# Kernel tuning notes

Hardware: AMD Instinct MI355X
Metric: run time of the kernel (lower is better)

The kernel has to match this reference:

```python
import jax, jax.numpy as jnp
import numpy as np

B, DIN, H, NACT = 8192, 1025, 1024, 1026
NHEAD = 513  # npatches + STOP
K = 32       # kR = kS


def _make_seq(key, batch, n, k):
    k_idx, k_len = jax.random.split(key)
    # distinct indices per row: top-k of a random permutation
    perm = jnp.argsort(jax.random.uniform(k_idx, (batch, n)), axis=1)[:, :k]
    seq_len = jax.random.randint(k_len, (batch,), 1, k + 1).astype(jnp.int32)
    mask = jnp.arange(k)[None, :] < seq_len[:, None]
    seq_idx = jnp.where(mask, perm, -1).astype(jnp.int32)
    return seq_idx, seq_len


def setup_inputs() -> dict:
    key = jax.random.key(0)
    ks = jax.random.split(key, 8)
    state = jax.random.normal(ks[0], (B, DIN), dtype=jnp.float32)
    W0 = jax.random.normal(ks[1], (DIN, H), dtype=jnp.float32) * (2.0 / DIN) ** 0.5
    b0 = jnp.zeros((H,), jnp.float32)
    W1 = jax.random.normal(ks[2], (H, H), dtype=jnp.float32) * (2.0 / H) ** 0.5
    b1 = jnp.zeros((H,), jnp.float32)
    W2 = jax.random.normal(ks[3], (H, NACT), dtype=jnp.float32) * 0.01
    b2 = jnp.zeros((NACT,), jnp.float32)
    seq_idx_R, seq_len_R = _make_seq(ks[4], B, NHEAD, K)
    seq_idx_S, seq_len_S = _make_seq(ks[5], B, NHEAD, K)
    return {"state": state, "W0": W0, "b0": b0, "W1": W1, "b1": b1,
            "W2": W2, "b2": b2,
            "seq_idx_R": seq_idx_R, "seq_len_R": seq_len_R,
            "seq_idx_S": seq_idx_S, "seq_len_S": seq_len_S}


def _mlp(state, W0, b0, W1, b1, W2, b2):
    h = jax.nn.relu(state @ W0 + b0)
    h = jax.nn.relu(h @ W1 + b1)
    return h @ W2 + b2  # (B, NACT) logits


def _logprob_entropy_wo_replacement(logits, seq_idx, seq_len):
    # Faithful vectorized version of logprob_entropy_wo_replacement_batched.
    bsz, n = logits.shape
    col = jnp.arange(n)[None, :]
    neg_inf = jnp.float32(-jnp.inf)

    def step(carry, xs):
        remaining, logp, ent = carry          # (B,N) bool, (B,), (B,)
        t, idx_t = xs                          # scalar, (B,)
        active = t < seq_len                   # (B,)
        masked_logits = jnp.where(remaining, logits, neg_inf)
        lp = jax.nn.log_softmax(masked_logits, axis=-1)
        p = jnp.exp(lp)
        mp = jnp.where(remaining, p, 0.0)
        mlp_ = jnp.where(remaining, lp, 0.0)
        ent_step = -jnp.sum(mp * mlp_, axis=-1)
        ent = ent + jnp.where(active, ent_step, 0.0)
        valid = active & (idx_t >= 0)
        idx_safe = jnp.where(valid, idx_t, 0)
        g = jnp.take_along_axis(lp, idx_safe[:, None], axis=1)[:, 0]
        logp = logp + jnp.where(valid, g, 0.0)
        hit = (col == idx_safe[:, None]) & valid[:, None]
        remaining = remaining & ~hit
        return (remaining, logp, ent), None

    init = (jnp.ones((bsz, n), bool), jnp.zeros((bsz,), jnp.float32),
            jnp.zeros((bsz,), jnp.float32))
    ts = jnp.arange(seq_idx.shape[1], dtype=jnp.int32)
    (_, logp, ent), _ = jax.lax.scan(step, init, (ts, seq_idx.T))
    return logp, ent


def reference(state, W0, b0, W1, b1, W2, b2,
              seq_idx_R, seq_len_R, seq_idx_S, seq_len_S):
    x = _mlp(state, W0, b0, W1, b1, W2, b2)
    logpR, entR = _logprob_entropy_wo_replacement(x[:, :NHEAD], seq_idx_R, seq_len_R)
    logpS, entS = _logprob_entropy_wo_replacement(x[:, NHEAD:NHEAD + NHEAD], seq_idx_S, seq_len_S)
    # rows: [total logprob, total entropy] as in get_log_prob's (logpR+logpS, entR+entS)
    return jnp.stack([logpR + logpS, entR + entS], axis=0)  # (2, B)
```

## Files before the change

kernel.cpp:

```cpp
#include <hip/hip_runtime.h>
#include <cstdint>
#include <cstddef>

#define BATCH 8192
#define DIN   1025
#define HID   1024
#define NACT  1026
#define NHEAD 513
#define KSEL  32
#define KP0   1088
#define LGN   1024

typedef unsigned short u16;
typedef short bf16x8 __attribute__((ext_vector_type(8)));
typedef float f32x4 __attribute__((ext_vector_type(4)));

__device__ __forceinline__ u16 f2bf(float f) {
  unsigned u = __float_as_uint(f);
  u += 0x7fff + ((u >> 16) & 1);
  return (u16)(u >> 16);
}
__device__ __forceinline__ float bf2f(u16 h) {
  return __uint_as_float((unsigned)h << 16);
}

__device__ __forceinline__ void async_cp16(const u16* g, u16* l) {
  __builtin_amdgcn_global_load_lds((const __attribute__((address_space(1))) void*)g,
                                   (__attribute__((address_space(3))) void*)l,
                                   16, 0, 0);
}

__global__ __launch_bounds__(512) void k_cvt(const float* __restrict__ state,
    const float* __restrict__ W0, const float* __restrict__ W1,
    const float* __restrict__ W2,
    u16* __restrict__ As, u16* __restrict__ W0t, u16* __restrict__ W1t,
    u16* __restrict__ W2t, u16* __restrict__ W2c) {
  const int tid = threadIdx.x;
  const int b = blockIdx.x;
  {
    int i = b * 512 + tid;
    const int QPR = KP0 / 4;
    int r = i / QPR, c4 = (i - r * QPR) * 4;
    const float* src = state + (size_t)r * DIN + c4;
    ushort4 o;
    if (c4 + 3 < DIN) {
      o.x = f2bf(src[0]); o.y = f2bf(src[1]); o.z = f2bf(src[2]); o.w = f2bf(src[3]);
    } else {
      o.x = (c4 + 0 < DIN) ? f2bf(src[0]) : 0;
      o.y = (c4 + 1 < DIN) ? f2bf(src[1]) : 0;
      o.z = (c4 + 2 < DIN) ? f2bf(src[2]) : 0;
      o.w = (c4 + 3 < DIN) ? f2bf(src[3]) : 0;
    }
    *(ushort4*)(As + (size_t)r * KP0 + c4) = o;
  }
  if (b >= 3137) return;
  if (b == 3136) {
    for (int e = tid; e < 2048; e += 512) {
      int j = e >> 10, k = e & 1023;
      W2c[e] = f2bf(W2[(size_t)k * NACT + 1024 + j]);
    }
    return;
  }
  const float* W; u16* Wt; int K, ldW, Kp, tt = b;
  if (tt < 1088)      { W = W0; Wt = W0t; K = DIN; ldW = HID;  Kp = KP0; }
  else if (tt < 2112) { tt -= 1088; W = W1; Wt = W1t; K = HID; ldW = HID;  Kp = HID; }
  else                { tt -= 2112; W = W2; Wt = W2t; K = HID; ldW = NACT; Kp = HID; }
  int n0 = (tt & 31) * 32, k0 = (tt >> 5) * 32;
  __shared__ float tile[32][33];
  const int tx = tid & 31, ty = tid >> 5;
#pragma unroll
  for (int i = 0; i < 32; i += 16) {
    int k = k0 + ty + i;
    tile[ty + i][tx] = (k < K) ? W[(size_t)k * ldW + n0 + tx] : 0.f;
  }
  __syncthreads();
#pragma unroll
  for (int i = 0; i < 32; i += 16)
    Wt[(size_t)(n0 + ty + i) * Kp + k0 + tx] = f2bf(tile[tx][ty + i]);
}

template<bool RELU, int K>
__global__ __launch_bounds__(256, 2)
void gemm_bt(const u16* __restrict__ A, const u16* __restrict__ Bt,
             const float* __restrict__ bias, u16* __restrict__ Cout, int ldc)
{
  __shared__ __align__(16) u16 lds[32768];

  const int d     = blockIdx.x;
  const int m8    = d & 7;
  const int ntile = (d >> 3) & 7;
  const int mtile = ((d >> 6) << 3) | m8;
  const size_t bm = (size_t)mtile * 128;
  const size_t bn = (size_t)ntile * 128;

  const int tid  = threadIdx.x;
  const int wave = tid >> 6;
  const int lane = tid & 63;
  const int waveM = wave >> 1, waveN = wave & 1;
  const int lr = lane & 15, lq = lane >> 4;

  const int row0 = tid >> 3;
  const int g_   = (tid & 7) ^ ((tid >> 3) & 7);
  const u16* gA0 = A  + (bm + row0)      * (size_t)K + g_ * 8;
  const u16* gA1 = A  + (bm + row0 + 32) * (size_t)K + g_ * 8;
  const u16* gA2 = A  + (bm + row0 + 64) * (size_t)K + g_ * 8;
  const u16* gA3 = A  + (bm + row0 + 96) * (size_t)K + g_ * 8;
  const u16* gB0 = Bt + (bn + row0)      * (size_t)K + g_ * 8;
  const u16* gB1 = Bt + (bn + row0 + 32) * (size_t)K + g_ * 8;
  const u16* gB2 = Bt + (bn + row0 + 64) * (size_t)K + g_ * 8;
  const u16* gB3 = Bt + (bn + row0 + 96) * (size_t)K + g_ * 8;
  u16* lA = lds + wave * 512;
  u16* lB = lds + 8192 + wave * 512;

  f32x4 acc[4][4] = {};

  const int xr  = lane & 7;
  const int sk0 = ((0 | lq) ^ xr) * 8;
  const int sk1 = ((4 | lq) ^ xr) * 8;
  const u16* pa = lds + (waveM * 64 + lr) * 64;
  const u16* pb = lds + 8192 + (waveN * 64 + lr) * 64;

  auto issue = [&](int k0, int buf) {
    const int o = buf * 16384;
    async_cp16(gA0 + k0, lA + o);
    async_cp16(gA1 + k0, lA + o + 2048);
    async_cp16(gA2 + k0, lA + o + 4096);
    async_cp16(gA3 + k0, lA + o + 6144);
    async_cp16(gB0 + k0, lB + o);
    async_cp16(gB1 + k0, lB + o + 2048);
    async_cp16(gB2 + k0, lB + o + 4096);
    async_cp16(gB3 + k0, lB + o + 6144);
  };

  const int NIT = K / 64;
  issue(0, 0);
#pragma unroll 2
  for (int it = 0; it < NIT; ++it) {
    const int buf = it & 1;
    if (it + 1 < NIT) {
      issue((it + 1) * 64, buf ^ 1);
      asm volatile("s_waitcnt vmcnt(8)\n\ts_barrier" ::: "memory");
    } else {
      asm volatile("s_waitcnt vmcnt(0)\n\ts_barrier" ::: "memory");
    }

    const u16* qa = pa + buf * 16384;
    const u16* qb = pb + buf * 16384;
    bf16x8 af[4], bfr[4];
#pragma unroll
    for (int t = 0; t < 4; ++t) {
      af[t]  = *(const bf16x8*)(qa + t * 1024 + sk0);
      bfr[t] = *(const bf16x8*)(qb + t * 1024 + sk0);
    }
#pragma unroll
    for (int tm = 0; tm < 4; ++tm)
#pragma unroll
      for (int tn = 0; tn < 4; ++tn)
        acc[tm][tn] = __builtin_amdgcn_mfma_f32_16x16x32_bf16(af[tm], bfr[tn], acc[tm][tn], 0, 0, 0);
#pragma unroll
    for (int t = 0; t < 4; ++t) {
      af[t]  = *(const bf16x8*)(qa + t * 1024 + sk1);
      bfr[t] = *(const bf16x8*)(qb + t * 1024 + sk1);
    }
#pragma unroll
    for (int tm = 0; tm < 4; ++tm)
#pragma unroll
      for (int tn = 0; tn < 4; ++tn)
        acc[tm][tn] = __builtin_amdgcn_mfma_f32_16x16x32_bf16(af[tm], bfr[tn], acc[tm][tn], 0, 0, 0);

    asm volatile("s_waitcnt lgkmcnt(0)\n\ts_barrier" ::: "memory");
  }

#pragma unroll
  for (int tm = 0; tm < 4; ++tm) {
    size_t rw = bm + waveM * 64 + tm * 16 + lq * 4;
#pragma unroll
    for (int tn = 0; tn < 4; ++tn) {
      int col = (int)bn + waveN * 64 + tn * 16 + lr;
      float bv = bias[col];
#pragma unroll
      for (int r = 0; r < 4; ++r) {
        float v = acc[tm][tn][r] + bv;
        if (RELU) v = fmaxf(v, 0.f);
        Cout[(rw + r) * ldc + col] = f2bf(v);
      }
    }
  }
}

__global__ __launch_bounds__(512) void k_sample(const u16* __restrict__ lgts,
    const u16* __restrict__ h2, const u16* __restrict__ W2c,
    const float* __restrict__ b2,
    const int* __restrict__ idxR, const int* __restrict__ lenR,
    const int* __restrict__ idxS, const int* __restrict__ lenS,
    float* __restrict__ out) {
  __shared__ float shf[16];
  const int tid = threadIdx.x;
  const int w = tid >> 6, lane = tid & 63;
  const int grp = w & 1, pair = w >> 1;
  const int row = blockIdx.x * 4 + pair;
  const u16* base = lgts + (size_t)row * LGN + (grp ? NHEAD : 0);
  const int* sidx = (grp ? idxS : idxR) + (size_t)row * KSEL;
  const int slen  = (grp ? lenS : lenR)[row];

  float x1024 = 0.f, x1025 = 0.f;
  if (grp) {
    const bf16x8* hp  = (const bf16x8*)(h2 + (size_t)row * HID + lane * 16);
    const bf16x8* w0p = (const bf16x8*)(W2c + lane * 16);
    const bf16x8* w1p = (const bf16x8*)(W2c + 1024 + lane * 16);
    bf16x8 hv0 = hp[0],  hv1 = hp[1];
    bf16x8 a0  = w0p[0], a1  = w0p[1];
    bf16x8 c0  = w1p[0], c1  = w1p[1];
    float d0 = 0.f, d1 = 0.f;
#pragma unroll
    for (int j = 0; j < 8; ++j) {
      float h0 = bf2f((u16)hv0[j]);
      float h1 = bf2f((u16)hv1[j]);
      d0 += h0 * bf2f((u16)a0[j]) + h1 * bf2f((u16)a1[j]);
      d1 += h0 * bf2f((u16)c0[j]) + h1 * bf2f((u16)c1[j]);
    }
#pragma unroll
    for (int dd = 32; dd; dd >>= 1) { d0 += __shfl_xor(d0, dd, 64); d1 += __shfl_xor(d1, dd, 64); }
    x1024 = d0 + b2[1024];
    x1025 = d1 + b2[1025];
  }

  const u16* chunk = lgts + (size_t)row * LGN + (grp ? 512 : 0) + lane * 8;
  bf16x8 raw = *(const bf16x8*)chunk;
  float v[8];
#pragma unroll
  for (int j = 0; j < 8; ++j) v[j] = bf2f((u16)raw[j]);
  if (grp && lane == 0) v[0] = -3.4e38f;

  float xa = -3.4e38f; int has_xa = 0;
  if (!grp && lane == 0)  { xa = bf2f(base[512]); has_xa = 1; }
  if (grp  && lane == 63) { xa = x1024;           has_xa = 1; }
  if (grp  && lane == 0)  { xa = x1025;           has_xa = 1; }

  float m = -3.4e38f;
#pragma unroll
  for (int j = 0; j < 8; ++j) m = fmaxf(m, v[j]);
  if (has_xa) m = fmaxf(m, xa);
#pragma unroll
  for (int dd = 32; dd; dd >>= 1) m = fmaxf(m, __shfl_xor(m, dd, 64));

  float S = 0.f, T = 0.f;
#pragma unroll
  for (int j = 0; j < 8; ++j) {
    float e = __expf(v[j] - m);
    S += e; T += e * v[j];
  }
  if (has_xa) { float e = __expf(xa - m); S += e; T += e * xa; }
#pragma unroll
  for (int dd = 32; dd; dd >>= 1) { S += __shfl_xor(S, dd, 64); T += __shfl_xor(T, dd, 64); }

  float e = 0.f, ex = 0.f, xt = 0.f;
  int active = (lane < KSEL) && (lane < slen);
  int valid = 0;
  if (active) {
    int id = sidx[lane];
    if (id >= 0) {
      valid = 1;
      if (grp && id >= 511) xt = (id == 511) ? x1024 : x1025;
      else                  xt = bf2f(base[id]);
      e  = __expf(xt - m);
      ex = e * xt;
    }
  }
  float pe = e, pex = ex;
#pragma unroll
  for (int dd = 1; dd < 32; dd <<= 1) {
    float qa = __shfl_up(pe, dd, 64);
    float qb = __shfl_up(pex, dd, 64);
    if (lane >= dd) { pe += qa; pex += qb; }
  }
  float lp = 0.f, en = 0.f;
  if (active) {
    float St = S - (pe - e);
    float Tt = T - (pex - ex);
    float logZ = m + __logf(St);
    en = logZ - Tt / St;
    if (valid) lp = xt - logZ;
  }
#pragma unroll
  for (int dd = 32; dd; dd >>= 1) { lp += __shfl_xor(lp, dd, 64); en += __shfl_xor(en, dd, 64); }

  if (lane == 0) { shf[w * 2] = lp; shf[w * 2 + 1] = en; }
  __syncthreads();
  if (lane == 0 && grp == 0) {
    out[row]         = shf[pair * 4] + shf[pair * 4 + 2];
    out[BATCH + row] = shf[pair * 4 + 1] + shf[pair * 4 + 3];
  }
}

extern "C" void kernel_launch(void* const* d_in, const int* in_sizes, int n_in,
                              void* d_out, int out_size, void* d_ws, size_t ws_size,
                              hipStream_t stream) {
  (void)in_sizes; (void)n_in; (void)out_size; (void)ws_size;
  const float* state = (const float*)d_in[0];
  const float* W0 = (const float*)d_in[1];
  const float* b0 = (const float*)d_in[2];
  const float* W1 = (const float*)d_in[3];
  const float* b1 = (const float*)d_in[4];
  const float* W2 = (const float*)d_in[5];
  const float* b2 = (const float*)d_in[6];
  const int* idxR = (const int*)d_in[7];
  const int* lenR = (const int*)d_in[8];
  const int* idxS = (const int*)d_in[9];
  const int* lenS = (const int*)d_in[10];
  float* out = (float*)d_out;

  char* ws = (char*)d_ws;
  size_t off = 0;
  auto alloc = [&](size_t bytes) -> char* {
    char* p = ws + off;
    off = (off + bytes + 255) & ~(size_t)255;
    return p;
  };
  u16* As   = (u16*)alloc((size_t)BATCH * KP0 * 2);
  u16* W0t  = (u16*)alloc((size_t)HID * KP0 * 2);
  u16* W1t  = (u16*)alloc((size_t)HID * HID * 2);
  u16* W2t  = (u16*)alloc((size_t)HID * LGN * 2);
  u16* W2c  = (u16*)alloc((size_t)2 * 1024 * 2);
  u16* h1   = (u16*)alloc((size_t)BATCH * HID * 2);
  u16* h2   = (u16*)alloc((size_t)BATCH * HID * 2);
  u16* lgts = (u16*)alloc((size_t)BATCH * LGN * 2);

  k_cvt<<<4352, 512, 0, stream>>>(state, W0, W1, W2, As, W0t, W1t, W2t, W2c);

  gemm_bt<true,  KP0><<<512, 256, 0, stream>>>(As, W0t, b0, h1,   HID);
  gemm_bt<true,  HID><<<512, 256, 0, stream>>>(h1, W1t, b1, h2,   HID);
  gemm_bt<false, HID><<<512, 256, 0, stream>>>(h2, W2t, b2, lgts, LGN);

  k_sample<<<2048, 512, 0, stream>>>(lgts, h2, W2c, b2, idxR, lenR, idxS, lenS, out);
}
```

Before: 178.9 us.

## Fuse three MLP GEMM launches into one persistent kernel with grid barriers

Replaces the three separate GEMM launches with one kernel that loops over the three layers and synchronises all 512 blocks through an atomic-counter grid barrier between layers. The counters are zeroed by the conversion kernel. The aim is to remove kernel launch gaps and tail drain between layers. It relies on all 512 blocks being co-resident (256 CUs at 2 blocks each), otherwise it deadlocks. It also loses compile-time K and the RELU template specialisation.

```diff
diff --git a/kernel.cpp b/kernel.cpp
--- a/kernel.cpp
+++ b/kernel.cpp
@@ -10,6 +10,7 @@
 #define KSEL  32
 #define KP0   1088
 #define LGN   1024
+#define GRIDM 512
 
 typedef unsigned short u16;
 typedef short bf16x8 __attribute__((ext_vector_type(8)));
@@ -30,11 +31,23 @@
                                    16, 0, 0);
 }
 
+__device__ __forceinline__ void grid_sync(unsigned* ctr) {
+  __syncthreads();
+  if (threadIdx.x == 0) {
+    __threadfence();
+    __hip_atomic_fetch_add(ctr, 1u, __ATOMIC_ACQ_REL, __HIP_MEMORY_SCOPE_AGENT);
+    while (__hip_atomic_load(ctr, __ATOMIC_ACQUIRE, __HIP_MEMORY_SCOPE_AGENT) < (unsigned)GRIDM)
+      __builtin_amdgcn_s_sleep(2);
+    __threadfence();
+  }
+  __syncthreads();
+}
+
 __global__ __launch_bounds__(512) void k_cvt(const float* __restrict__ state,
     const float* __restrict__ W0, const float* __restrict__ W1,
     const float* __restrict__ W2,
     u16* __restrict__ As, u16* __restrict__ W0t, u16* __restrict__ W1t,
-    u16* __restrict__ W2t, u16* __restrict__ W2c) {
+    u16* __restrict__ W2t, u16* __restrict__ W2c, unsigned* __restrict__ gbar) {
   const int tid = threadIdx.x;
   const int b = blockIdx.x;
   {
@@ -53,6 +66,7 @@
     }
     *(ushort4*)(As + (size_t)r * KP0 + c4) = o;
   }
+  if (b == 4351 && tid < 8) gbar[tid] = 0;
   if (b >= 3137) return;
   if (b == 3136) {
     for (int e = tid; e < 2048; e += 512) {
@@ -79,10 +93,13 @@
     Wt[(size_t)(n0 + ty + i) * Kp + k0 + tx] = f2bf(tile[tx][ty + i]);
 }
 
-template<bool RELU, int K>
 __global__ __launch_bounds__(256, 2)
-void gemm_bt(const u16* __restrict__ A, const u16* __restrict__ Bt,
-             const float* __restrict__ bias, u16* __restrict__ Cout, int ldc)
+void k_mlp(const u16* __restrict__ As, const u16* __restrict__ W0t,
+           const float* __restrict__ b0, u16* __restrict__ h1,
+           const u16* __restrict__ W1t, const float* __restrict__ b1,
+           u16* __restrict__ h2,
+           const u16* __restrict__ W2t, const float* __restrict__ b2v,
+           u16* __restrict__ lgts, unsigned* __restrict__ gbar)
 {
   __shared__ __align__(16) u16 lds[32768];
 
@@ -101,18 +118,8 @@
 
   const int row0 = tid >> 3;
   const int g_   = (tid & 7) ^ ((tid >> 3) & 7);
-  const u16* gA0 = A  + (bm + row0)      * (size_t)K + g_ * 8;
-  const u16* gA1 = A  + (bm + row0 + 32) * (size_t)K + g_ * 8;
-  const u16* gA2 = A  + (bm + row0 + 64) * (size_t)K + g_ * 8;
-  const u16* gA3 = A  + (bm + row0 + 96) * (size_t)K + g_ * 8;
-  const u16* gB0 = Bt + (bn + row0)      * (size_t)K + g_ * 8;
-  const u16* gB1 = Bt + (bn + row0 + 32) * (size_t)K + g_ * 8;
-  const u16* gB2 = Bt + (bn + row0 + 64) * (size_t)K + g_ * 8;
-  const u16* gB3 = Bt + (bn + row0 + 96) * (size_t)K + g_ * 8;
   u16* lA = lds + wave * 512;
   u16* lB = lds + 8192 + wave * 512;
-
-  f32x4 acc[4][4] = {};
 
   const int xr  = lane & 7;
   const int sk0 = ((0 | lq) ^ xr) * 8;
@@ -120,71 +127,91 @@
   const u16* pa = lds + (waveM * 64 + lr) * 64;
   const u16* pb = lds + 8192 + (waveN * 64 + lr) * 64;
 
-  auto issue = [&](int k0, int buf) {
-    const int o = buf * 16384;
-    async_cp16(gA0 + k0, lA + o);
-    async_cp16(gA1 + k0, lA + o + 2048);
-    async_cp16(gA2 + k0, lA + o + 4096);
-    async_cp16(gA3 + k0, lA + o + 6144);
-    async_cp16(gB0 + k0, lB + o);
-    async_cp16(gB1 + k0, lB + o + 2048);
-    async_cp16(gB2 + k0, lB + o + 4096);
-    async_cp16(gB3 + k0, lB + o + 6144);
-  };
-
-  const int NIT = K / 64;
-  issue(0, 0);
+  for (int layer = 0; layer < 3; ++layer) {
+    const u16 *A, *Bt; const float* bias; u16* C; int K, ldc, relu;
+    if (layer == 0)      { A = As; Bt = W0t; bias = b0;  C = h1;   K = KP0; ldc = HID; relu = 1; }
+    else if (layer == 1) { A = h1; Bt = W1t; bias = b1;  C = h2;   K = HID; ldc = HID; relu = 1; }
+    else                 { A = h2; Bt = W2t; bias = b2v; C = lgts; K = HID; ldc = LGN; relu = 0; }
+
+    const u16* gA0 = A  + (bm + row0)      * (size_t)K + g_ * 8;
+    const u16* gA1 = A  + (bm + row0 + 32) * (size_t)K + g_ * 8;
+    const u16* gA2 = A  + (bm + row0 + 64) * (size_t)K + g_ * 8;
+    const u16* gA3 = A  + (bm + row0 + 96) * (size_t)K + g_ * 8;
+    const u16* gB0 = Bt + (bn + row0)      * (size_t)K + g_ * 8;
+    const u16* gB1 = Bt + (bn + row0 + 32) * (size_t)K + g_ * 8;
+    const u16* gB2 = Bt + (bn + row0 + 64) * (size_t)K + g_ * 8;
+    const u16* gB3 = Bt + (bn + row0 + 96) * (size_t)K + g_ * 8;
+
+    f32x4 acc[4][4] = {};
+
+    auto issue = [&](int k0, int buf) {
+      const int o = buf * 16384;
+      async_cp16(gA0 + k0, lA + o);
+      async_cp16(gA1 + k0, lA + o + 2048);
+      async_cp16(gA2 + k0, lA + o + 4096);
+      async_cp16(gA3 + k0, lA + o + 6144);
+      async_cp16(gB0 + k0, lB + o);
+      async_cp16(gB1 + k0, lB + o + 2048);
+      async_cp16(gB2 + k0, lB + o + 4096);
+      async_cp16(gB3 + k0, lB + o + 6144);
+    };
+
+    const int NIT = K / 64;
+    issue(0, 0);
 #pragma unroll 2
-  for (int it = 0; it < NIT; ++it) {
-    const int buf = it & 1;
-    if (it + 1 < NIT) {
-      issue((it + 1) * 64, buf ^ 1);
-      asm volatile("s_waitcnt vmcnt(8)\n\ts_barrier" ::: "memory");
-    } else {
-      asm volatile("s_waitcnt vmcnt(0)\n\ts_barrier" ::: "memory");
-    }
-
-    const u16* qa = pa + buf * 16384;
-    const u16* qb = pb + buf * 16384;
-    bf16x8 af[4], bfr[4];
-#pragma unroll
-    for (int t = 0; t < 4; ++t) {
-      af[t]  = *(const bf16x8*)(qa + t * 1024 + sk0);
-      bfr[t] = *(const bf16x8*)(qb + t * 1024 + sk0);
-    }
-#pragma unroll
-    for (int tm = 0; tm < 4; ++tm)
-#pragma unroll
-      for (int tn = 0; tn < 4; ++tn)
-        acc[tm][tn] = __builtin_amdgcn_mfma_f32_16x16x32_bf16(af[tm], bfr[tn], acc[tm][tn], 0, 0, 0);
-#pragma unroll
-    for (int t = 0; t < 4; ++t) {
-      af[t]  = *(const bf16x8*)(qa + t * 1024 + sk1);
-      bfr[t] = *(const bf16x8*)(qb + t * 1024 + sk1);
-    }
-#pragma unroll
-    for (int tm = 0; tm < 4; ++tm)
-#pragma unroll
-      for (int tn = 0; tn < 4; ++tn)
-        acc[tm][tn] = __builtin_amdgcn_mfma_f32_16x16x32_bf16(af[tm], bfr[tn], acc[tm][tn], 0, 0, 0);
-
-    asm volatile("s_waitcnt lgkmcnt(0)\n\ts_barrier" ::: "memory");
-  }
-
-#pragma unroll
-  for (int tm = 0; tm < 4; ++tm) {
-    size_t rw = bm + waveM * 64 + tm * 16 + lq * 4;
-#pragma unroll
-    for (int tn = 0; tn < 4; ++tn) {
-      int col = (int)bn + waveN * 64 + tn * 16 + lr;
-      float bv = bias[col];
-#pragma unroll
-      for (int r = 0; r < 4; ++r) {
-        float v = acc[tm][tn][r] + bv;
-        if (RELU) v = fmaxf(v, 0.f);
-        Cout[(rw + r) * ldc + col] = f2bf(v);
+    for (int it = 0; it < NIT; ++it) {
+      const int buf = it & 1;
+      if (it + 1 < NIT) {
+        issue((it + 1) * 64, buf ^ 1);
+        asm volatile("s_waitcnt vmcnt(8)\n\ts_barrier" ::: "memory");
+      } else {
+        asm volatile("s_waitcnt vmcnt(0)\n\ts_barrier" ::: "memory");
       }
-    }
+
+      const u16* qa = pa + buf * 16384;
+      const u16* qb = pb + buf * 16384;
+      bf16x8 af[4], bfr[4];
+#pragma unroll
+      for (int t = 0; t < 4; ++t) {
+        af[t]  = *(const bf16x8*)(qa + t * 1024 + sk0);
+        bfr[t] = *(const bf16x8*)(qb + t * 1024 + sk0);
+      }
+#pragma unroll
+      for (int tm = 0; tm < 4; ++tm)
+#pragma unroll
+        for (int tn = 0; tn < 4; ++tn)
+          acc[tm][tn] = __builtin_amdgcn_mfma_f32_16x16x32_bf16(af[tm], bfr[tn], acc[tm][tn], 0, 0, 0);
+#pragma unroll
+      for (int t = 0; t < 4; ++t) {
+        af[t]  = *(const bf16x8*)(qa + t * 1024 + sk1);
+        bfr[t] = *(const bf16x8*)(qb + t * 1024 + sk1);
+      }
+#pragma unroll
+      for (int tm = 0; tm < 4; ++tm)
+#pragma unroll
+        for (int tn = 0; tn < 4; ++tn)
+          acc[tm][tn] = __builtin_amdgcn_mfma_f32_16x16x32_bf16(af[tm], bfr[tn], acc[tm][tn], 0, 0, 0);
+
+      asm volatile("s_waitcnt lgkmcnt(0)\n\ts_barrier" ::: "memory");
+    }
+
+#pragma unroll
+    for (int tm = 0; tm < 4; ++tm) {
+      size_t rw = bm + waveM * 64 + tm * 16 + lq * 4;
+#pragma unroll
+      for (int tn = 0; tn < 4; ++tn) {
+        int col = (int)bn + waveN * 64 + tn * 16 + lr;
+        float bv = bias[col];
+#pragma unroll
+        for (int r = 0; r < 4; ++r) {
+          float v = acc[tm][tn][r] + bv;
+          if (relu) v = fmaxf(v, 0.f);
+          C[(rw + r) * (size_t)ldc + col] = f2bf(v);
+        }
+      }
+    }
+
+    if (layer < 2) grid_sync(gbar + layer);
   }
 }
 
@@ -325,12 +352,11 @@
   u16* h1   = (u16*)alloc((size_t)BATCH * HID * 2);
   u16* h2   = (u16*)alloc((size_t)BATCH * HID * 2);
   u16* lgts = (u16*)alloc((size_t)BATCH * LGN * 2);
-
-  k_cvt<<<4352, 512, 0, stream>>>(state, W0, W1, W2, As, W0t, W1t, W2t, W2c);
-
-  gemm_bt<true,  KP0><<<512, 256, 0, stream>>>(As, W0t, b0, h1,   HID);
-  gemm_bt<true,  HID><<<512, 256, 0, stream>>>(h1, W1t, b1, h2,   HID);
-  gemm_bt<false, HID><<<512, 256, 0, stream>>>(h2, W2t, b2, lgts, LGN);
+  unsigned* gbar = (unsigned*)alloc(256);
+
+  k_cvt<<<4352, 512, 0, stream>>>(state, W0, W1, W2, As, W0t, W1t, W2t, W2c, gbar);
+
+  k_mlp<<<GRIDM, 256, 0, stream>>>(As, W0t, b0, h1, W1t, b1, h2, W2t, b2, lgts, gbar);
 
   k_sample<<<2048, 512, 0, stream>>>(lgts, h2, W2c, b2, idxR, lenR, idxS, lenS, out);
 }
```

Measured after the change: 360.9 us. +101.7%, slower.
